# Kernel optimization log

Measured on AMD Instinct MI355X. Metric: run time of the kernel, lower is better.

The kernel has to match this reference:

```python
import jax, jax.numpy as jnp
import numpy as np

B, L_Q, S_KV, H, E = 4, 1024, 1024, 8, 64
IN_CH = OUT_CH = 512
MODES = 64
INDEX_Q = np.arange(MODES)   # 'lowest' mode selection -> range(0, modes)
INDEX_KV = np.arange(MODES)
SCALE = 1.0 / np.sqrt(OUT_CH)
FACTOR = 5


def setup_inputs() -> dict:
    key = jax.random.key(0)
    ks = jax.random.split(key, 7)
    tf_queries = jax.random.normal(ks[0], (B, L_Q, H, E), jnp.float32)
    queries = jax.random.normal(ks[1], (B, L_Q, H, E), jnp.float32)
    keys = jax.random.normal(ks[2], (B, S_KV, H, E), jnp.float32)
    values = jax.random.normal(ks[3], (B, S_KV, H, E), jnp.float32)
    mask = jnp.ones((1,), jnp.int32)  # unused by the module
    weights_fuse = jax.random.uniform(ks[4], (H, L_Q, 2), jnp.float32)
    # torch.rand with cfloat dtype samples re/im independently from U[0,1)
    w1_re = SCALE * jax.random.uniform(ks[5], (H, IN_CH // 8, OUT_CH // 8, MODES), jnp.float32)
    w1_im = SCALE * jax.random.uniform(ks[6], (H, IN_CH // 8, OUT_CH // 8, MODES), jnp.float32)
    return dict(tf_queries=tf_queries, queries=queries, keys=keys, values=values,
                mask=mask, weights_fuse=weights_fuse, w1_re=w1_re, w1_im=w1_im)


def get_sig_scores(n, queries, keys, scale, corr):
    # queries/keys: [B, L, H, E] (keys already aligned to L_Q)
    B_, Lq, H_, E_ = queries.shape
    Lk = keys.shape[1]
    q = jnp.transpose(queries, (0, 2, 1, 3))  # [B,H,L,E]
    k = jnp.transpose(keys, (0, 2, 1, 3))
    if corr:
        qf = jnp.fft.rfft(jnp.transpose(queries, (0, 2, 3, 1)), axis=-1)
        kf = jnp.fft.rfft(jnp.transpose(keys, (0, 2, 3, 1)), axis=-1)
        autocorr = jnp.transpose(jnp.fft.irfft(qf * jnp.conj(kf), axis=-1), (0, 1, 3, 2))  # [B,H,L,E]
    else:
        autocorr = q
    amp = jnp.linalg.norm(autocorr, axis=-1)           # [B,H,L]
    _, top_idx = jax.lax.top_k(amp, n)                 # [B,H,n]
    q_sel = jnp.take_along_axis(q, top_idx[..., None], axis=2)  # [B,H,n,E]
    scores = jnp.einsum('bhnd,bhmd->bhnm', q_sel, k) * scale    # [B,H,n,Lk]
    full = jnp.full((B_, H_, Lq, Lk), -jnp.inf, scores.dtype)
    bi = jnp.arange(B_)[:, None, None]
    hi = jnp.arange(H_)[None, :, None]
    full = full.at[bi, hi, top_idx].set(scores)        # scatter selected query rows
    # softmax over the query axis for every key position (transpose(2,3))
    return jax.nn.softmax(jnp.swapaxes(full, 2, 3), axis=-1)  # [B,H,Lk,Lq]


def reference(tf_queries, queries, keys, values, mask, weights_fuse, w1_re, w1_im):
    B_, Lq, H_, E_ = queries.shape
    S_ = keys.shape[1]
    xq = jnp.transpose(queries, (0, 2, 3, 1))  # [B,H,E,L_Q]
    xk = jnp.transpose(keys, (0, 2, 3, 1))     # [B,H,E,S]
    if Lq > S_:
        pad = jnp.zeros((B_, Lq - S_, H_, E_), keys.dtype)
        keys2 = jnp.concatenate([keys, pad], axis=1)
        values2 = jnp.concatenate([values, pad], axis=1)
    else:
        keys2 = keys[:, :Lq]
        values2 = values[:, :Lq]
    n_top = min(int(FACTOR * np.ceil(np.log(Lq))), Lq)

    attn_t = get_sig_scores(n_top, queries, keys2, SCALE, corr=True)
    attn_tf = get_sig_scores(n_top, tf_queries, keys2, SCALE, corr=False)

    nw = jax.nn.softmax(weights_fuse, axis=-1)  # [H,L_Q,2]
    fused = nw[None, :, :, 0, None] * attn_t + nw[None, :, :, 1, None] * attn_tf
    # dropout(p=0.1) in eval mode -> identity

    xq_ft = jnp.fft.rfft(xq, axis=-1)[:, :, :, INDEX_Q]   # [B,H,E,M]
    xk_ft = jnp.fft.rfft(xk, axis=-1)[:, :, :, INDEX_KV]  # [B,H,E,M]
    xqk = jnp.tanh(jnp.einsum('bhex,bhey->bhxy', xq_ft, xk_ft))  # complex tanh
    xqkv = jnp.einsum('bhxy,bhey->bhex', xqk, xk_ft)
    w1 = w1_re + 1j * w1_im
    xqkvw = jnp.einsum('bhex,heox->bhox', xqkv, w1)        # [B,H,O,M]
    out_ft = jnp.zeros((B_, H_, E_, Lq // 2 + 1), xqkvw.dtype)
    out_ft = out_ft.at[:, :, :, INDEX_Q].set(xqkvw)
    out = jnp.fft.irfft(out_ft / IN_CH / OUT_CH, n=Lq, axis=-1)  # [B,H,E,L_Q]

    output = jnp.einsum('bhlm,bhmd->bhld', fused, jnp.transpose(values2, (0, 2, 1, 3)))
    output = jnp.transpose(output, (0, 1, 3, 2))  # [B,H,D,L_Q]
    return (output + out) * 0.5
```

## Files before the change

kernel.cpp:

```cpp
#include <hip/hip_runtime.h>
#include <math.h>

#define B_ 4
#define H_ 8
#define L_ 1024
#define E_ 64
#define NTOP 35
#define SCALE_ 0.04419417382415922f

__global__ __launch_bounds__(256) void k_stage(const float* __restrict__ q_g,
                                               const float* __restrict__ k_g,
                                               float* __restrict__ xtq,
                                               float* __restrict__ xtk) {
  __shared__ float tile[64][65];
  const int tc = blockIdx.x & 15;
  const int src = (blockIdx.x >> 4) & 1;
  const int bh = blockIdx.x >> 5;
  const int b = bh >> 3, h = bh & 7;
  const int t0 = tc * 64;
  const int tid = threadIdx.x;
  const float* in = src ? k_g : q_g;
  float* out = src ? xtk : xtq;

  for (int idx = tid; idx < 1024; idx += 256) {
    int t = idx >> 4, e4 = idx & 15;
    float4 v = reinterpret_cast<const float4*>(
        in + ((size_t)(b * L_ + t0 + t) * H_ + h) * E_)[e4];
    tile[t][e4 * 4 + 0] = v.x; tile[t][e4 * 4 + 1] = v.y;
    tile[t][e4 * 4 + 2] = v.z; tile[t][e4 * 4 + 3] = v.w;
  }
  __syncthreads();
  for (int idx = tid; idx < 1024; idx += 256) {
    int e = idx >> 4, t4 = idx & 15;
    float4 v = make_float4(tile[t4 * 4 + 0][e], tile[t4 * 4 + 1][e],
                           tile[t4 * 4 + 2][e], tile[t4 * 4 + 3][e]);
    reinterpret_cast<float4*>(out + ((size_t)(bh * 64 + e)) * 1024 + t0)[t4] = v;
  }
}

__global__ __launch_bounds__(512) void k_fft_c(const float* __restrict__ xtq,
                                               const float* __restrict__ xtk,
                                               float* __restrict__ amp2_part,
                                               float* __restrict__ qft,
                                               float* __restrict__ kft) {
  __shared__ __align__(16) float zre[4][1024], zim[4][1024];
  __shared__ float ctab[512], stab[512];
  const int eg = blockIdx.x & 15;
  const int bh = blockIdx.x >> 4;
  const int tid = threadIdx.x;
  const float TWO_PI_N = 6.283185307179586f / 1024.0f;

  if (tid < 512) {
    float s, c;
    sincosf(TWO_PI_N * (float)tid, &s, &c);
    ctab[tid] = c; stab[tid] = s;
  }
  for (int idx = tid; idx < 1024; idx += 512) {
    int ee = idx >> 8, t4 = idx & 255;
    size_t ro = ((size_t)(bh * 64 + eg * 4 + ee)) * 1024;
    float4 qv = reinterpret_cast<const float4*>(xtq + ro)[t4];
    float4 kv = reinterpret_cast<const float4*>(xtk + ro)[t4];
    *reinterpret_cast<float4*>(&zre[ee][t4 * 4]) = qv;
    *reinterpret_cast<float4*>(&zim[ee][t4 * 4]) = kv;
  }
  __syncthreads();

  for (int s = 0; s < 10; ++s) {
    const int half = 512 >> s;
#pragma unroll
    for (int it = 0; it < 4; ++it) {
      int idx = tid + it * 512;
      int ee = idx >> 9;
      int bf = idx & 511;
      int j = bf & (half - 1);
      int p0 = ((bf >> (9 - s)) << (10 - s)) + j;
      int p1 = p0 + half;
      float ur = zre[ee][p0], ui = zim[ee][p0];
      float vr = zre[ee][p1], vi = zim[ee][p1];
      float dr = ur - vr, di = ui - vi;
      zre[ee][p0] = ur + vr; zim[ee][p0] = ui + vi;
      int twi = j << s;
      float c = ctab[twi], sn = stab[twi];
      zre[ee][p1] = fmaf(dr, c, di * sn);
      zim[ee][p1] = fmaf(di, c, -dr * sn);
    }
    __syncthreads();
  }

  float pr[8], pi_[8];
#pragma unroll
  for (int it = 0; it < 8; ++it) {
    int idx = tid + it * 512;
    int ee = idx >> 10;
    int p = idx & 1023;
    int m = __brev((unsigned)p) >> 22;
    int mp = (1024 - m) & 1023;
    int pp = __brev((unsigned)mp) >> 22;
    float ar = zre[ee][p], ai = zim[ee][p];
    float br = zre[ee][pp], bi = zim[ee][pp];
    float qr = 0.5f * (ar + br), qi = 0.5f * (ai - bi);
    float kr = 0.5f * (ai + bi), ki = -0.5f * (ar - br);
    pr[it]  = fmaf(qr, kr, qi * ki);
    pi_[it] = fmaf(qi, kr, -qr * ki);
    if (m < 64) {
      size_t o = ((size_t)(bh * 64 + eg * 4 + ee) * 64 + m) * 2;
      qft[o] = qr; qft[o + 1] = qi;
      kft[o] = kr; kft[o + 1] = ki;
    }
  }
  __syncthreads();
#pragma unroll
  for (int it = 0; it < 8; ++it) {
    int idx = tid + it * 512;
    int ee = idx >> 10;
    int p = idx & 1023;
    zre[ee][p] = pr[it]; zim[ee][p] = pi_[it];
  }
  __syncthreads();

  for (int idx = tid; idx < 2048; idx += 512) {
    int u = idx >> 10;
    int p = idx & 1023;
    int e0 = 2 * u, e1 = 2 * u + 1;
    float s_r = zre[e0][p] - zim[e1][p];
    float s_i = zim[e0][p] + zre[e1][p];
    zre[e0][p] = s_r; zim[e0][p] = s_i;
  }
  __syncthreads();

  for (int s = 9; s >= 0; --s) {
    const int half = 512 >> s;
#pragma unroll
    for (int it = 0; it < 2; ++it) {
      int idx = tid + it * 512;
      int ee = (idx >> 9) * 2;
      int bf = idx & 511;
      int j = bf & (half - 1);
      int p0 = ((bf >> (9 - s)) << (10 - s)) + j;
      int p1 = p0 + half;
      int twi = j << s;
      float c = ctab[twi], sn = stab[twi];
      float ur = zre[ee][p0], ui = zim[ee][p0];
      float wr = zre[ee][p1], wi = zim[ee][p1];
      float vr = fmaf(wr, c, -wi * sn);
      float vi = fmaf(wi, c, wr * sn);
      zre[ee][p0] = ur + vr; zim[ee][p0] = ui + vi;
      zre[ee][p1] = ur - vr; zim[ee][p1] = ui - vi;
    }
    __syncthreads();
  }

  for (int t = tid; t < 1024; t += 512) {
    float r0 = zre[0][t], i0 = zim[0][t];
    float r2 = zre[2][t], i2 = zim[2][t];
    amp2_part[(size_t)(bh * 16 + eg) * 1024 + t] =
        fmaf(r0, r0, fmaf(i0, i0, fmaf(r2, r2, i2 * i2)));
  }
}

__global__ __launch_bounds__(256) void k_fft_s(const float* __restrict__ q_g,
                                               const float* __restrict__ k_g,
                                               float* __restrict__ amp2_part,
                                               float* __restrict__ qft,
                                               float* __restrict__ kft) {
  __shared__ float zre[4][1024], zim[4][1024];
  __shared__ float ctab[512], stab[512];
  const int eg = blockIdx.x & 15;
  const int bh = blockIdx.x >> 4;
  const int b = bh >> 3, h = bh & 7;
  const int tid = threadIdx.x;
  const float TWO_PI_N = 6.283185307179586f / 1024.0f;

  for (int j = tid; j < 512; j += 256) {
    float s, c;
    sincosf(TWO_PI_N * (float)j, &s, &c);
    ctab[j] = c; stab[j] = s;
  }
  for (int t = tid; t < 1024; t += 256) {
    size_t g4 = ((size_t)(b * L_ + t) * H_ + h) * 16 + eg;
    float4 qv = reinterpret_cast<const float4*>(q_g)[g4];
    float4 kv = reinterpret_cast<const float4*>(k_g)[g4];
    zre[0][t] = qv.x; zre[1][t] = qv.y; zre[2][t] = qv.z; zre[3][t] = qv.w;
    zim[0][t] = kv.x; zim[1][t] = kv.y; zim[2][t] = kv.z; zim[3][t] = kv.w;
  }
  __syncthreads();

  for (int s = 0; s < 10; ++s) {
    const int half = 512 >> s;
#pragma unroll
    for (int it = 0; it < 8; ++it) {
      int idx = tid + it * 256;
      int ee = idx >> 9;
      int bf = idx & 511;
      int j = bf & (half - 1);
      int p0 = ((bf >> (9 - s)) << (10 - s)) + j;
      int p1 = p0 + half;
      float ur = zre[ee][p0], ui = zim[ee][p0];
      float vr = zre[ee][p1], vi = zim[ee][p1];
      float dr = ur - vr, di = ui - vi;
      zre[ee][p0] = ur + vr; zim[ee][p0] = ui + vi;
      int twi = j << s;
      float c = ctab[twi], sn = stab[twi];
      zre[ee][p1] = fmaf(dr, c, di * sn);
      zim[ee][p1] = fmaf(di, c, -dr * sn);
    }
    __syncthreads();
  }

  float pr[16], pi_[16];
#pragma unroll
  for (int it = 0; it < 16; ++it) {
    int idx = tid + it * 256;
    int ee = idx >> 10;
    int p = idx & 1023;
    int m = __brev((unsigned)p) >> 22;
    int mp = (1024 - m) & 1023;
    int pp = __brev((unsigned)mp) >> 22;
    float ar = zre[ee][p], ai = zim[ee][p];
    float br = zre[ee][pp], bi = zim[ee][pp];
    float qr = 0.5f * (ar + br), qi = 0.5f * (ai - bi);
    float kr = 0.5f * (ai + bi), ki = -0.5f * (ar - br);
    pr[it]  = fmaf(qr, kr, qi * ki);
    pi_[it] = fmaf(qi, kr, -qr * ki);
    if (m < 64) {
      size_t o = ((size_t)(bh * 64 + eg * 4 + ee) * 64 + m) * 2;
      qft[o] = qr; qft[o + 1] = qi;
      kft[o] = kr; kft[o + 1] = ki;
    }
  }
  __syncthreads();
#pragma unroll
  for (int it = 0; it < 16; ++it) {
    int idx = tid + it * 256;
    int ee = idx >> 10;
    int p = idx & 1023;
    zre[ee][p] = pr[it]; zim[ee][p] = pi_[it];
  }
  __syncthreads();

  for (int idx = tid; idx < 2048; idx += 256) {
    int u = idx >> 10;
    int p = idx & 1023;
    int e0 = 2 * u, e1 = 2 * u + 1;
    float s_r = zre[e0][p] - zim[e1][p];
    float s_i = zim[e0][p] + zre[e1][p];
    zre[e0][p] = s_r; zim[e0][p] = s_i;
  }
  __syncthreads();

  for (int s = 9; s >= 0; --s) {
    const int half = 512 >> s;
#pragma unroll
    for (int it = 0; it < 4; ++it) {
      int idx = tid + it * 256;
      int ee = (idx >> 9) * 2;
      int bf = idx & 511;
      int j = bf & (half - 1);
      int p0 = ((bf >> (9 - s)) << (10 - s)) + j;
      int p1 = p0 + half;
      int twi = j << s;
      float c = ctab[twi], sn = stab[twi];
      float ur = zre[ee][p0], ui = zim[ee][p0];
      float wr = zre[ee][p1], wi = zim[ee][p1];
      float vr = fmaf(wr, c, -wi * sn);
      float vi = fmaf(wi, c, wr * sn);
      zre[ee][p0] = ur + vr; zim[ee][p0] = ui + vi;
      zre[ee][p1] = ur - vr; zim[ee][p1] = ui - vi;
    }
    __syncthreads();
  }

  for (int t = tid; t < 1024; t += 256) {
    float r0 = zre[0][t], i0 = zim[0][t];
    float r2 = zre[2][t], i2 = zim[2][t];
    amp2_part[(size_t)(bh * 16 + eg) * 1024 + t] =
        fmaf(r0, r0, fmaf(i0, i0, fmaf(r2, r2, i2 * i2)));
  }
}

__global__ __launch_bounds__(256) void k_red(const float* __restrict__ amp2_part,
                                             const float* __restrict__ tfq,
                                             float* __restrict__ ampsum) {
  const int blk = blockIdx.x;
  const int tid = threadIdx.x;
  if (blk < 32) {
    const int bh = blk;
    for (int t = tid; t < 1024; t += 256) {
      float s = 0.f;
#pragma unroll
      for (int c = 0; c < 16; ++c)
        s += amp2_part[(size_t)(bh * 16 + c) * 1024 + t];
      ampsum[(size_t)(bh * 2) * 1024 + t] = s;
    }
  } else {
    const int idx = blk - 32;
    const int bh = idx >> 2, qt = idx & 3;
    const int b = bh >> 3, h = bh & 7;
    const int l = qt * 256 + tid;
    const float4* p4 = reinterpret_cast<const float4*>(
        &tfq[((size_t)(b * L_ + l) * H_ + h) * E_]);
    float s = 0.f;
#pragma unroll
    for (int e4 = 0; e4 < 16; ++e4) {
      float4 v = p4[e4];
      s += v.x * v.x + v.y * v.y + v.z * v.z + v.w * v.w;
    }
    ampsum[(size_t)(bh * 2 + 1) * 1024 + l] = s;
  }
}

__global__ __launch_bounds__(64) void k_sel(const float* __restrict__ ampsum,
                                            int* __restrict__ sel_ws) {
  const int p = blockIdx.x;
  const int lane = threadIdx.x;
  float val[16];
#pragma unroll
  for (int j = 0; j < 16; ++j)
    val[j] = ampsum[(size_t)p * 1024 + j * 64 + lane];

  float bv = -1.f; int bi = lane;
#pragma unroll
  for (int j = 0; j < 16; ++j) {
    if (val[j] > bv) { bv = val[j]; bi = j * 64 + lane; }
  }

  for (int it = 0; it < NTOP; ++it) {
    float v = bv; int i = bi;
#pragma unroll
    for (int d = 1; d < 64; d <<= 1) {
      float ov = __shfl_xor(v, d);
      int oi = __shfl_xor(i, d);
      if (ov > v || (ov == v && oi < i)) { v = ov; i = oi; }
    }
    if (lane == 0) sel_ws[p * 64 + it] = i;
    if ((i & 63) == lane) {
      int jr = i >> 6;
#pragma unroll
      for (int j = 0; j < 16; ++j) if (j == jr) val[j] = -1.f;
      bv = -1.f; bi = lane;
#pragma unroll
      for (int j = 0; j < 16; ++j) {
        if (val[j] > bv) { bv = val[j]; bi = j * 64 + lane; }
      }
    }
  }
}

__global__ __launch_bounds__(256) void k_topk(const float* __restrict__ amp2_part,
                                              const float* __restrict__ tfq,
                                              int* __restrict__ sel_ws) {
  __shared__ float amp[1024];
  __shared__ float wv_s[4];
  __shared__ int wi_s[4];
  __shared__ int winner_s;
  const int src = blockIdx.x & 1;
  const int bh = blockIdx.x >> 1;
  const int b = bh >> 3, h = bh & 7;
  const int tid = threadIdx.x;

  if (src == 0) {
    for (int t = tid; t < 1024; t += 256) {
      float s = 0.f;
#pragma unroll
      for (int c = 0; c < 16; ++c) s += amp2_part[(size_t)(bh * 16 + c) * 1024 + t];
      amp[t] = s;
    }
  } else {
    for (int l = tid; l < 1024; l += 256) {
      const float4* p4 = reinterpret_cast<const float4*>(
          &tfq[((size_t)(b * L_ + l) * H_ + h) * E_]);
      float s = 0.f;
#pragma unroll
      for (int e4 = 0; e4 < 16; ++e4) {
        float4 v = p4[e4];
        s += v.x * v.x + v.y * v.y + v.z * v.z + v.w * v.w;
      }
      amp[l] = s;
    }
  }
  __syncthreads();

  float bv = -1.f; int bi = tid;
#pragma unroll
  for (int kk = 0; kk < 4; ++kk) {
    int t = tid + kk * 256;
    float v = amp[t];
    if (v > bv) { bv = v; bi = t; }
  }
  const int lane = tid & 63, w = tid >> 6;

  for (int it = 0; it < NTOP; ++it) {
    float v = bv; int i = bi;
#pragma unroll
    for (int d = 1; d < 64; d <<= 1) {
      float ov = __shfl_xor(v, d);
      int oi = __shfl_xor(i, d);
      if (ov > v || (ov == v && oi < i)) { v = ov; i = oi; }
    }
    if (lane == 0) { wv_s[w] = v; wi_s[w] = i; }
    __syncthreads();
    if (tid == 0) {
      float fv = wv_s[0]; int fi = wi_s[0];
#pragma unroll
      for (int j = 1; j < 4; ++j) {
        if (wv_s[j] > fv || (wv_s[j] == fv && wi_s[j] < fi)) { fv = wv_s[j]; fi = wi_s[j]; }
      }
      winner_s = fi;
      sel_ws[(bh * 2 + src) * 64 + it] = fi;
    }
    __syncthreads();
    int fi = winner_s;
    if ((fi & 255) == tid) {
      amp[fi] = -1.f;
      bv = -1.f; bi = tid;
#pragma unroll
      for (int kk = 0; kk < 4; ++kk) {
        int t = tid + kk * 256;
        float vv = amp[t];
        if (vv > bv) { bv = vv; bi = t; }
      }
    }
  }
}

__global__ __launch_bounds__(256) void k_attn(const float* __restrict__ q_g,
                                              const float* __restrict__ tfq,
                                              const float* __restrict__ k_g,
                                              const float* __restrict__ v_g,
                                              const float* __restrict__ wfuse,
                                              const int* __restrict__ sel_ws,
                                              float* __restrict__ out) {
  __shared__ float4 qs4[2][NTOP][16];
  __shared__ float4 vs4[2][NTOP][16];
  const int ac = blockIdx.x & 15;
  const int bh = blockIdx.x >> 4;
  const int b = bh >> 3, h = bh & 7;
  const int a0 = ac * 64;
  const int tid = threadIdx.x;

  for (int idx = tid; idx < 2 * NTOP * 16; idx += 256) {
    int src = idx / (NTOP * 16);
    int rem = idx - src * (NTOP * 16);
    int i = rem >> 4, e4 = rem & 15;
    int row = sel_ws[(bh * 2 + src) * 64 + i];
    size_t rb = ((size_t)(b * L_ + row) * H_ + h) * E_;
    const float* qbase = src ? tfq : q_g;
    qs4[src][i][e4] = reinterpret_cast<const float4*>(qbase + rb)[e4];
    vs4[src][i][e4] = reinterpret_cast<const float4*>(v_g + rb)[e4];
  }
  __syncthreads();

  const int qd = tid & 3, r = tid >> 2;
  const int a = a0 + r;
  const int eb = qd * 16;

  size_t krb = ((size_t)(b * L_ + a) * H_ + h) * E_;
  const float4* k4p = reinterpret_cast<const float4*>(k_g + krb);
  float4 kq[4];
#pragma unroll
  for (int j4 = 0; j4 < 4; ++j4) kq[j4] = k4p[qd * 4 + j4];

  float ct[NTOP], ctf[NTOP];
#pragma unroll
  for (int i = 0; i < NTOP; ++i) { ct[i] = 0.f; ctf[i] = 0.f; }

#pragma unroll
  for (int j4 = 0; j4 < 4; ++j4) {
    float4 kv = kq[j4];
#pragma unroll
    for (int i = 0; i < NTOP; ++i) {
      float4 q4 = qs4[0][i][qd * 4 + j4];
      ct[i] = fmaf(q4.x, kv.x, ct[i]); ct[i] = fmaf(q4.y, kv.y, ct[i]);
      ct[i] = fmaf(q4.z, kv.z, ct[i]); ct[i] = fmaf(q4.w, kv.w, ct[i]);
      float4 p4 = qs4[1][i][qd * 4 + j4];
      ctf[i] = fmaf(p4.x, kv.x, ctf[i]); ctf[i] = fmaf(p4.y, kv.y, ctf[i]);
      ctf[i] = fmaf(p4.z, kv.z, ctf[i]); ctf[i] = fmaf(p4.w, kv.w, ctf[i]);
    }
  }
#pragma unroll
  for (int i = 0; i < NTOP; ++i) {
    ct[i] += __shfl_xor(ct[i], 1);  ct[i] += __shfl_xor(ct[i], 2);
    ctf[i] += __shfl_xor(ctf[i], 1); ctf[i] += __shfl_xor(ctf[i], 2);
  }

  float wf0 = wfuse[(h * L_ + a) * 2 + 0];
  float wf1 = wfuse[(h * L_ + a) * 2 + 1];
  float wm = fmaxf(wf0, wf1);
  float ew0 = expf(wf0 - wm), ew1 = expf(wf1 - wm);
  float nw0 = ew0 / (ew0 + ew1), nw1 = ew1 / (ew0 + ew1);

  {
    float m = -1e30f;
#pragma unroll
    for (int i = 0; i < NTOP; ++i) { ct[i] *= SCALE_; m = fmaxf(m, ct[i]); }
    float sum = 0.f;
#pragma unroll
    for (int i = 0; i < NTOP; ++i) { ct[i] = expf(ct[i] - m); sum += ct[i]; }
    float c = 0.5f * nw0 / sum;
#pragma unroll
    for (int i = 0; i < NTOP; ++i) ct[i] *= c;
  }
  {
    float m = -1e30f;
#pragma unroll
    for (int i = 0; i < NTOP; ++i) { ctf[i] *= SCALE_; m = fmaxf(m, ctf[i]); }
    float sum = 0.f;
#pragma unroll
    for (int i = 0; i < NTOP; ++i) { ctf[i] = expf(ctf[i] - m); sum += ctf[i]; }
    float c = 0.5f * nw1 / sum;
#pragma unroll
    for (int i = 0; i < NTOP; ++i) ctf[i] *= c;
  }
#pragma unroll
  for (int j4 = 0; j4 < 4; ++j4) {
    float ax = 0.f, ay = 0.f, az = 0.f, aw = 0.f;
#pragma unroll
    for (int i = 0; i < NTOP; ++i) {
      float4 v4 = vs4[0][i][qd * 4 + j4];
      ax = fmaf(ct[i], v4.x, ax); ay = fmaf(ct[i], v4.y, ay);
      az = fmaf(ct[i], v4.z, az); aw = fmaf(ct[i], v4.w, aw);
    }
#pragma unroll
    for (int i = 0; i < NTOP; ++i) {
      float4 v4 = vs4[1][i][qd * 4 + j4];
      ax = fmaf(ctf[i], v4.x, ax); ay = fmaf(ctf[i], v4.y, ay);
      az = fmaf(ctf[i], v4.z, az); aw = fmaf(ctf[i], v4.w, aw);
    }
    int d = eb + j4 * 4;
    out[((size_t)(bh * 64 + d + 0)) * 1024 + a] = ax;
    out[((size_t)(bh * 64 + d + 1)) * 1024 + a] = ay;
    out[((size_t)(bh * 64 + d + 2)) * 1024 + a] = az;
    out[((size_t)(bh * 64 + d + 3)) * 1024 + a] = aw;
  }
}

__global__ __launch_bounds__(256) void k_spec12(const float* __restrict__ qft,
                                                 const float* __restrict__ kft,
                                                 float* __restrict__ xre_g,
                                                 float* __restrict__ xim_g) {
  __shared__ float kre[64][65], kim[64][65];
  __shared__ float qre[64][8], qim[64][8];
  __shared__ float tre[8][64], tim[8][64];
  const int xc = blockIdx.x & 7;
  const int bh = blockIdx.x >> 3;
  const int tid = threadIdx.x;

  for (int idx = tid; idx < 4096; idx += 256) {
    int e = idx >> 6, y = idx & 63;
    size_t o = ((size_t)(bh * 64 + e) * 64 + y) * 2;
    kre[e][y] = kft[o]; kim[e][y] = kft[o + 1];
  }
  for (int idx = tid; idx < 512; idx += 256) {
    int e = idx >> 3, xl = idx & 7;
    size_t o = ((size_t)(bh * 64 + e) * 64 + xc * 8 + xl) * 2;
    qre[e][xl] = qft[o]; qim[e][xl] = qft[o + 1];
  }
  __syncthreads();

  const int y = tid & 63, xg = tid >> 6;
#pragma unroll
  for (int xi = 0; xi < 2; ++xi) {
    int xl = xg + xi * 4;
    float ar = 0.f, ai = 0.f;
    for (int e = 0; e < 64; ++e) {
      float a = qre[e][xl], b = qim[e][xl];
      float c = kre[e][y], d = kim[e][y];
      ar = fmaf(a, c, fmaf(-b, d, ar));
      ai = fmaf(a, d, fmaf(b, c, ai));
    }
    float trv, tiv;
    float x2 = 2.f * ar, y2 = 2.f * ai;
    if (fabsf(x2) > 30.f) {
      trv = copysignf(1.f, ar); tiv = 0.f;
    } else {
      float sh = sinhf(x2), ch = coshf(x2);
      float sn = sinf(y2), cs = cosf(y2);
      float dd = ch + cs;
      trv = sh / dd; tiv = sn / dd;
    }
    tre[xl][y] = trv; tim[xl][y] = tiv;
  }
  __syncthreads();

  const int e2 = tid & 63, xg2 = tid >> 6;
#pragma unroll
  for (int xi = 0; xi < 2; ++xi) {
    int xl = xg2 + xi * 4;
    float ar = 0.f, ai = 0.f;
    for (int yy = 0; yy < 64; ++yy) {
      float a = tre[xl][yy], b = tim[xl][yy];
      float c = kre[e2][yy], d = kim[e2][yy];
      ar = fmaf(a, c, fmaf(-b, d, ar));
      ai = fmaf(a, d, fmaf(b, c, ai));
    }
    xre_g[(size_t)bh * 4096 + (xc * 8 + xl) * 64 + e2] = ar;
    xim_g[(size_t)bh * 4096 + (xc * 8 + xl) * 64 + e2] = ai;
  }
}

__global__ __launch_bounds__(256) void k_w1(const float* __restrict__ xre_g,
                                            const float* __restrict__ xim_g,
                                            const float* __restrict__ w1re,
                                            const float* __restrict__ w1im,
                                            float* __restrict__ xw) {
  __shared__ float xre[64][65], xim[64][65];
  __shared__ float redr[4][512], redi[4][512];
  const int oc = blockIdx.x & 7;
  const int bh = blockIdx.x >> 3;
  const int h = bh & 7;
  const int tid = threadIdx.x;

  for (int idx = tid; idx < 4096; idx += 256) {
    int x = idx >> 6, e = idx & 63;
    xre[e][x] = xre_g[(size_t)bh * 4096 + idx];
    xim[e][x] = xim_g[(size_t)bh * 4096 + idx];
  }
  __syncthreads();

  const int x = tid & 63, g = tid >> 6;
  float accr[8], acci[8];
#pragma unroll
  for (int oo = 0; oo < 8; ++oo) { accr[oo] = 0.f; acci[oo] = 0.f; }

  for (int ee = 0; ee < 16; ++ee) {
    int e = g * 16 + ee;
    float a = xre[e][x], b = xim[e][x];
    size_t wbase = (((size_t)h * 64 + e) * 64 + oc * 8) * 64 + x;
#pragma unroll
    for (int oo = 0; oo < 8; ++oo) {
      float c = w1re[wbase + (size_t)oo * 64];
      float d = w1im[wbase + (size_t)oo * 64];
      accr[oo] = fmaf(a, c, fmaf(-b, d, accr[oo]));
      acci[oo] = fmaf(a, d, fmaf(b, c, acci[oo]));
    }
  }
#pragma unroll
  for (int oo = 0; oo < 8; ++oo) {
    redr[g][oo * 64 + x] = accr[oo];
    redi[g][oo * 64 + x] = acci[oo];
  }
  __syncthreads();

  const float INV = 1.0f / (512.0f * 512.0f);
  for (int idx = tid; idx < 512; idx += 256) {
    int oo = idx >> 6, x2 = idx & 63;
    float r = redr[0][idx] + redr[1][idx] + redr[2][idx] + redr[3][idx];
    float i = redi[0][idx] + redi[1][idx] + redi[2][idx] + redi[3][idx];
    size_t oidx = ((size_t)(bh * 64 + oc * 8 + oo) * 64 + x2) * 2;
    xw[oidx] = r * INV;
    xw[oidx + 1] = i * INV;
  }
}

__global__ __launch_bounds__(256) void k_final(const float* __restrict__ xw,
                                               float* __restrict__ out) {
  __shared__ float Xre[8][64], Xim[8][64];
  const int tc = blockIdx.x & 3;
  const int oc = (blockIdx.x >> 2) & 7;
  const int bh = blockIdx.x >> 5;
  const int o0 = oc * 8;
  const int tid = threadIdx.x;

  for (int idx = tid; idx < 512; idx += 256) {
    int o = idx >> 6, m = idx & 63;
    size_t s = ((size_t)(bh * 64 + o0 + o) * 64 + m) * 2;
    Xre[o][m] = 2.f * xw[s]; Xim[o][m] = 2.f * xw[s + 1];
  }
  __syncthreads();

  const int t = tc * 256 + tid;
  const float HALF_INVN = 0.5f / 1024.0f;
  const float TWO_PI = 6.283185307179586f;
  float th = TWO_PI * (float)t * (1.0f / 1024.0f);
  float s1, c1;
  __sincosf(th, &s1, &c1);
  float cm = c1, sm = s1;

  float acc[8];
#pragma unroll
  for (int o = 0; o < 8; ++o) acc[o] = 0.5f * Xre[o][0];

  for (int m = 1; m < 64; ++m) {
#pragma unroll
    for (int o = 0; o < 8; ++o) {
      acc[o] = fmaf(Xre[o][m], cm, acc[o]);
      acc[o] = fmaf(-Xim[o][m], sm, acc[o]);
    }
    float cn = fmaf(cm, c1, -sm * s1);
    float sn = fmaf(sm, c1, cm * s1);
    cm = cn; sm = sn;
  }
#pragma unroll
  for (int o = 0; o < 8; ++o) {
    size_t oi = ((size_t)(bh * 64 + o0 + o)) * 1024 + t;
    out[oi] = fmaf(acc[o], HALF_INVN, out[oi]);
  }
}

extern "C" void kernel_launch(void* const* d_in, const int* in_sizes, int n_in,
                              void* d_out, int out_size, void* d_ws, size_t ws_size,
                              hipStream_t stream) {
  const float* tfq   = (const float*)d_in[0];
  const float* q     = (const float*)d_in[1];
  const float* k     = (const float*)d_in[2];
  const float* v     = (const float*)d_in[3];
  const float* wfuse = (const float*)d_in[5];
  const float* w1re  = (const float*)d_in[6];
  const float* w1im  = (const float*)d_in[7];
  float* out = (float*)d_out;
  float* ws  = (float*)d_ws;

  const size_t STAGED_FLOATS = 5312512;
  if (ws_size >= STAGED_FLOATS * sizeof(float)) {
    float* xtq    = ws;
    float* xtk    = ws + 2097152;
    float* amp2   = ws + 4194304;
    float* qft    = ws + 4718592;
    float* kft    = ws + 4980736;
    int*   sel    = (int*)(ws + 5242880);
    float* ampsum = ws + 5246976;
    float* xre_g  = ws;
    float* xim_g  = ws + 131072;
    float* xw     = ws + 262144;

    k_stage<<<1024, 256, 0, stream>>>(q, k, xtq, xtk);
    k_fft_c<<<512, 512, 0, stream>>>(xtq, xtk, amp2, qft, kft);
    k_red<<<160, 256, 0, stream>>>(amp2, tfq, ampsum);
    k_sel<<<64, 64, 0, stream>>>(ampsum, sel);
    k_attn<<<512, 256, 0, stream>>>(q, tfq, k, v, wfuse, sel, out);
    k_spec12<<<256, 256, 0, stream>>>(qft, kft, xre_g, xim_g);
    k_w1<<<256, 256, 0, stream>>>(xre_g, xim_g, w1re, w1im, xw);
    k_final<<<1024, 256, 0, stream>>>(xw, out);
  } else {
    float* amp2  = ws;
    float* xre_g = ws;
    float* xim_g = ws + 131072;
    float* xw    = ws + 262144;
    float* qft   = ws + 524288;
    float* kft   = ws + 786432;
    int*   sel   = (int*)(ws + 1048576);

    k_fft_s<<<512, 256, 0, stream>>>(q, k, amp2, qft, kft);
    k_topk<<<64, 256, 0, stream>>>(amp2, tfq, sel);
    k_attn<<<512, 256, 0, stream>>>(q, tfq, k, v, wfuse, sel, out);
    k_spec12<<<256, 256, 0, stream>>>(qft, kft, xre_g, xim_g);
    k_w1<<<256, 256, 0, stream>>>(xre_g, xim_g, w1re, w1im, xw);
    k_final<<<1024, 256, 0, stream>>>(xw, out);
  }
}
```

Measured before the change: 134.0 us.

## Merge independent stages into five launches via virtual-block dispatch

Kernel bodies become device functions that take a virtual block id and a shared scratch buffer. Independent stages then share one launch: staging runs with the tfq norm, the amp reduction and top-k run with spec12, and attention runs with the w1 projection. The launch count in the staged path drops from eight to five, which cuts launch gaps and lets independent work fill the GPU together. In exchange, each fused launch reserves shared memory for its largest stage, which may lower occupancy for the smaller stages.

Result: faster. 114.0 us (-14.9%).

```diff
diff --git a/kernel.cpp b/kernel.cpp
--- a/kernel.cpp
+++ b/kernel.cpp
@@ -8,14 +8,16 @@
 #define NTOP 35
 #define SCALE_ 0.04419417382415922f
 
-__global__ __launch_bounds__(256) void k_stage(const float* __restrict__ q_g,
-                                               const float* __restrict__ k_g,
-                                               float* __restrict__ xtq,
-                                               float* __restrict__ xtk) {
-  __shared__ float tile[64][65];
-  const int tc = blockIdx.x & 15;
-  const int src = (blockIdx.x >> 4) & 1;
-  const int bh = blockIdx.x >> 5;
+
+__device__ __forceinline__ void dev_stage(char* smem, int vbid,
+                                          const float* __restrict__ q_g,
+                                          const float* __restrict__ k_g,
+                                          float* __restrict__ xtq,
+                                          float* __restrict__ xtk) {
+  float* tile = reinterpret_cast<float*>(smem);
+  const int tc = vbid & 15;
+  const int src = (vbid >> 4) & 1;
+  const int bh = vbid >> 5;
   const int b = bh >> 3, h = bh & 7;
   const int t0 = tc * 64;
   const int tid = threadIdx.x;
@@ -26,27 +28,47 @@
     int t = idx >> 4, e4 = idx & 15;
     float4 v = reinterpret_cast<const float4*>(
         in + ((size_t)(b * L_ + t0 + t) * H_ + h) * E_)[e4];
-    tile[t][e4 * 4 + 0] = v.x; tile[t][e4 * 4 + 1] = v.y;
-    tile[t][e4 * 4 + 2] = v.z; tile[t][e4 * 4 + 3] = v.w;
+    tile[t * 65 + e4 * 4 + 0] = v.x; tile[t * 65 + e4 * 4 + 1] = v.y;
+    tile[t * 65 + e4 * 4 + 2] = v.z; tile[t * 65 + e4 * 4 + 3] = v.w;
   }
   __syncthreads();
   for (int idx = tid; idx < 1024; idx += 256) {
     int e = idx >> 4, t4 = idx & 15;
-    float4 v = make_float4(tile[t4 * 4 + 0][e], tile[t4 * 4 + 1][e],
-                           tile[t4 * 4 + 2][e], tile[t4 * 4 + 3][e]);
+    float4 v = make_float4(tile[(t4 * 4 + 0) * 65 + e], tile[(t4 * 4 + 1) * 65 + e],
+                           tile[(t4 * 4 + 2) * 65 + e], tile[(t4 * 4 + 3) * 65 + e]);
     reinterpret_cast<float4*>(out + ((size_t)(bh * 64 + e)) * 1024 + t0)[t4] = v;
   }
 }
 
-__global__ __launch_bounds__(512) void k_fft_c(const float* __restrict__ xtq,
-                                               const float* __restrict__ xtk,
-                                               float* __restrict__ amp2_part,
-                                               float* __restrict__ qft,
-                                               float* __restrict__ kft) {
-  __shared__ __align__(16) float zre[4][1024], zim[4][1024];
-  __shared__ float ctab[512], stab[512];
-  const int eg = blockIdx.x & 15;
-  const int bh = blockIdx.x >> 4;
+__device__ __forceinline__ void dev_tfqnorm(int vbid,
+                                            const float* __restrict__ tfq,
+                                            float* __restrict__ ampsum) {
+  const int bh = vbid >> 2, qt = vbid & 3;
+  const int b = bh >> 3, h = bh & 7;
+  const int l = qt * 256 + threadIdx.x;
+  const float4* p4 = reinterpret_cast<const float4*>(
+      &tfq[((size_t)(b * L_ + l) * H_ + h) * E_]);
+  float s = 0.f;
+#pragma unroll
+  for (int e4 = 0; e4 < 16; ++e4) {
+    float4 v = p4[e4];
+    s += v.x * v.x + v.y * v.y + v.z * v.z + v.w * v.w;
+  }
+  ampsum[(size_t)(bh * 2 + 1) * 1024 + l] = s;
+}
+
+__device__ __forceinline__ void dev_fft(char* smem, int vbid,
+                                        const float* __restrict__ xtq,
+                                        const float* __restrict__ xtk,
+                                        float* __restrict__ amp2_part,
+                                        float* __restrict__ qft,
+                                        float* __restrict__ kft) {
+  float* zre = reinterpret_cast<float*>(smem);
+  float* zim = zre + 4096;
+  float* ctab = zim + 4096;
+  float* stab = ctab + 512;
+  const int eg = vbid & 15;
+  const int bh = vbid >> 4;
   const int tid = threadIdx.x;
   const float TWO_PI_N = 6.283185307179586f / 1024.0f;
 
@@ -60,8 +82,8 @@
     size_t ro = ((size_t)(bh * 64 + eg * 4 + ee)) * 1024;
     float4 qv = reinterpret_cast<const float4*>(xtq + ro)[t4];
     float4 kv = reinterpret_cast<const float4*>(xtk + ro)[t4];
-    *reinterpret_cast<float4*>(&zre[ee][t4 * 4]) = qv;
-    *reinterpret_cast<float4*>(&zim[ee][t4 * 4]) = kv;
+    *reinterpret_cast<float4*>(&zre[ee * 1024 + t4 * 4]) = qv;
+    *reinterpret_cast<float4*>(&zim[ee * 1024 + t4 * 4]) = kv;
   }
   __syncthreads();
 
@@ -75,14 +97,14 @@
       int j = bf & (half - 1);
       int p0 = ((bf >> (9 - s)) << (10 - s)) + j;
       int p1 = p0 + half;
-      float ur = zre[ee][p0], ui = zim[ee][p0];
-      float vr = zre[ee][p1], vi = zim[ee][p1];
+      float ur = zre[ee * 1024 + p0], ui = zim[ee * 1024 + p0];
+      float vr = zre[ee * 1024 + p1], vi = zim[ee * 1024 + p1];
       float dr = ur - vr, di = ui - vi;
-      zre[ee][p0] = ur + vr; zim[ee][p0] = ui + vi;
+      zre[ee * 1024 + p0] = ur + vr; zim[ee * 1024 + p0] = ui + vi;
       int twi = j << s;
       float c = ctab[twi], sn = stab[twi];
-      zre[ee][p1] = fmaf(dr, c, di * sn);
-      zim[ee][p1] = fmaf(di, c, -dr * sn);
+      zre[ee * 1024 + p1] = fmaf(dr, c, di * sn);
+      zim[ee * 1024 + p1] = fmaf(di, c, -dr * sn);
     }
     __syncthreads();
   }
@@ -96,8 +118,8 @@
     int m = __brev((unsigned)p) >> 22;
     int mp = (1024 - m) & 1023;
     int pp = __brev((unsigned)mp) >> 22;
-    float ar = zre[ee][p], ai = zim[ee][p];
-    float br = zre[ee][pp], bi = zim[ee][pp];
+    float ar = zre[ee * 1024 + p], ai = zim[ee * 1024 + p];
+    float br = zre[ee * 1024 + pp], bi = zim[ee * 1024 + pp];
     float qr = 0.5f * (ar + br), qi = 0.5f * (ai - bi);
     float kr = 0.5f * (ai + bi), ki = -0.5f * (ar - br);
     pr[it]  = fmaf(qr, kr, qi * ki);
@@ -114,7 +136,7 @@
     int idx = tid + it * 512;
     int ee = idx >> 10;
     int p = idx & 1023;
-    zre[ee][p] = pr[it]; zim[ee][p] = pi_[it];
+    zre[ee * 1024 + p] = pr[it]; zim[ee * 1024 + p] = pi_[it];
   }
   __syncthreads();
 
@@ -122,9 +144,9 @@
     int u = idx >> 10;
     int p = idx & 1023;
     int e0 = 2 * u, e1 = 2 * u + 1;
-    float s_r = zre[e0][p] - zim[e1][p];
-    float s_i = zim[e0][p] + zre[e1][p];
-    zre[e0][p] = s_r; zim[e0][p] = s_i;
+    float s_r = zre[e0 * 1024 + p] - zim[e1 * 1024 + p];
+    float s_i = zim[e0 * 1024 + p] + zre[e1 * 1024 + p];
+    zre[e0 * 1024 + p] = s_r; zim[e0 * 1024 + p] = s_i;
   }
   __syncthreads();
 
@@ -140,23 +162,421 @@
       int p1 = p0 + half;
       int twi = j << s;
       float c = ctab[twi], sn = stab[twi];
-      float ur = zre[ee][p0], ui = zim[ee][p0];
-      float wr = zre[ee][p1], wi = zim[ee][p1];
+      float ur = zre[ee * 1024 + p0], ui = zim[ee * 1024 + p0];
+      float wr = zre[ee * 1024 + p1], wi = zim[ee * 1024 + p1];
       float vr = fmaf(wr, c, -wi * sn);
       float vi = fmaf(wi, c, wr * sn);
-      zre[ee][p0] = ur + vr; zim[ee][p0] = ui + vi;
-      zre[ee][p1] = ur - vr; zim[ee][p1] = ui - vi;
+      zre[ee * 1024 + p0] = ur + vr; zim[ee * 1024 + p0] = ui + vi;
+      zre[ee * 1024 + p1] = ur - vr; zim[ee * 1024 + p1] = ui - vi;
     }
     __syncthreads();
   }
 
   for (int t = tid; t < 1024; t += 512) {
-    float r0 = zre[0][t], i0 = zim[0][t];
-    float r2 = zre[2][t], i2 = zim[2][t];
+    float r0 = zre[t], i0 = zim[t];
+    float r2 = zre[2 * 1024 + t], i2 = zim[2 * 1024 + t];
     amp2_part[(size_t)(bh * 16 + eg) * 1024 + t] =
         fmaf(r0, r0, fmaf(i0, i0, fmaf(r2, r2, i2 * i2)));
   }
 }
+
+__device__ __forceinline__ void dev_sel(char* smem, int vbid,
+                                        const float* __restrict__ amp2_part,
+                                        const float* __restrict__ ampsum,
+                                        int* __restrict__ sel_ws) {
+  float* amp = reinterpret_cast<float*>(smem);
+  const int p = vbid;
+  const int tid = threadIdx.x;
+
+  if ((p & 1) == 0) {
+    const int bh = p >> 1;
+    for (int t = tid; t < 1024; t += 256) {
+      float s = 0.f;
+#pragma unroll
+      for (int c = 0; c < 16; ++c)
+        s += amp2_part[(size_t)(bh * 16 + c) * 1024 + t];
+      amp[t] = s;
+    }
+  } else {
+    for (int t = tid; t < 1024; t += 256)
+      amp[t] = ampsum[(size_t)p * 1024 + t];
+  }
+  __syncthreads();
+
+  if (tid < 64) {
+    const int lane = tid;
+    float val[16];
+#pragma unroll
+    for (int j = 0; j < 16; ++j) val[j] = amp[j * 64 + lane];
+
+    float bv = -1.f; int bi = lane;
+#pragma unroll
+    for (int j = 0; j < 16; ++j) {
+      if (val[j] > bv) { bv = val[j]; bi = j * 64 + lane; }
+    }
+    for (int it = 0; it < NTOP; ++it) {
+      float v = bv; int i = bi;
+#pragma unroll
+      for (int d = 1; d < 64; d <<= 1) {
+        float ov = __shfl_xor(v, d);
+        int oi = __shfl_xor(i, d);
+        if (ov > v || (ov == v && oi < i)) { v = ov; i = oi; }
+      }
+      if (lane == 0) sel_ws[p * 64 + it] = i;
+      if ((i & 63) == lane) {
+        int jr = i >> 6;
+#pragma unroll
+        for (int j = 0; j < 16; ++j) if (j == jr) val[j] = -1.f;
+        bv = -1.f; bi = lane;
+#pragma unroll
+        for (int j = 0; j < 16; ++j) {
+          if (val[j] > bv) { bv = val[j]; bi = j * 64 + lane; }
+        }
+      }
+    }
+  }
+}
+
+__device__ __forceinline__ void dev_attn(char* smem, int vbid,
+                                         const float* __restrict__ q_g,
+                                         const float* __restrict__ tfq,
+                                         const float* __restrict__ k_g,
+                                         const float* __restrict__ v_g,
+                                         const float* __restrict__ wfuse,
+                                         const int* __restrict__ sel_ws,
+                                         float* __restrict__ out) {
+  float4* qs4 = reinterpret_cast<float4*>(smem);
+  float4* vs4 = qs4 + 2 * NTOP * 16;
+  const int ac = vbid & 15;
+  const int bh = vbid >> 4;
+  const int b = bh >> 3, h = bh & 7;
+  const int a0 = ac * 64;
+  const int tid = threadIdx.x;
+
+  for (int idx = tid; idx < 2 * NTOP * 16; idx += 256) {
+    int src = idx / (NTOP * 16);
+    int rem = idx - src * (NTOP * 16);
+    int i = rem >> 4, e4 = rem & 15;
+    int row = sel_ws[(bh * 2 + src) * 64 + i];
+    size_t rb = ((size_t)(b * L_ + row) * H_ + h) * E_;
+    const float* qbase = src ? tfq : q_g;
+    qs4[(src * NTOP + i) * 16 + e4] = reinterpret_cast<const float4*>(qbase + rb)[e4];
+    vs4[(src * NTOP + i) * 16 + e4] = reinterpret_cast<const float4*>(v_g + rb)[e4];
+  }
+  __syncthreads();
+
+  const int qd = tid & 3, r = tid >> 2;
+  const int a = a0 + r;
+  const int eb = qd * 16;
+
+  size_t krb = ((size_t)(b * L_ + a) * H_ + h) * E_;
+  const float4* k4p = reinterpret_cast<const float4*>(k_g + krb);
+  float4 kq[4];
+#pragma unroll
+  for (int j4 = 0; j4 < 4; ++j4) kq[j4] = k4p[qd * 4 + j4];
+
+  float ct[NTOP], ctf[NTOP];
+#pragma unroll
+  for (int i = 0; i < NTOP; ++i) { ct[i] = 0.f; ctf[i] = 0.f; }
+
+#pragma unroll
+  for (int j4 = 0; j4 < 4; ++j4) {
+    float4 kv = kq[j4];
+#pragma unroll
+    for (int i = 0; i < NTOP; ++i) {
+      float4 q4 = qs4[(0 * NTOP + i) * 16 + qd * 4 + j4];
+      ct[i] = fmaf(q4.x, kv.x, ct[i]); ct[i] = fmaf(q4.y, kv.y, ct[i]);
+      ct[i] = fmaf(q4.z, kv.z, ct[i]); ct[i] = fmaf(q4.w, kv.w, ct[i]);
+      float4 p4 = qs4[(1 * NTOP + i) * 16 + qd * 4 + j4];
+      ctf[i] = fmaf(p4.x, kv.x, ctf[i]); ctf[i] = fmaf(p4.y, kv.y, ctf[i]);
+      ctf[i] = fmaf(p4.z, kv.z, ctf[i]); ctf[i] = fmaf(p4.w, kv.w, ctf[i]);
+    }
+  }
+#pragma unroll
+  for (int i = 0; i < NTOP; ++i) {
+    ct[i] += __shfl_xor(ct[i], 1);  ct[i] += __shfl_xor(ct[i], 2);
+    ctf[i] += __shfl_xor(ctf[i], 1); ctf[i] += __shfl_xor(ctf[i], 2);
+  }
+
+  float wf0 = wfuse[(h * L_ + a) * 2 + 0];
+  float wf1 = wfuse[(h * L_ + a) * 2 + 1];
+  float wm = fmaxf(wf0, wf1);
+  float ew0 = expf(wf0 - wm), ew1 = expf(wf1 - wm);
+  float nw0 = ew0 / (ew0 + ew1), nw1 = ew1 / (ew0 + ew1);
+
+  {
+    float m = -1e30f;
+#pragma unroll
+    for (int i = 0; i < NTOP; ++i) { ct[i] *= SCALE_; m = fmaxf(m, ct[i]); }
+    float sum = 0.f;
+#pragma unroll
+    for (int i = 0; i < NTOP; ++i) { ct[i] = expf(ct[i] - m); sum += ct[i]; }
+    float c = 0.5f * nw0 / sum;
+#pragma unroll
+    for (int i = 0; i < NTOP; ++i) ct[i] *= c;
+  }
+  {
+    float m = -1e30f;
+#pragma unroll
+    for (int i = 0; i < NTOP; ++i) { ctf[i] *= SCALE_; m = fmaxf(m, ctf[i]); }
+    float sum = 0.f;
+#pragma unroll
+    for (int i = 0; i < NTOP; ++i) { ctf[i] = expf(ctf[i] - m); sum += ctf[i]; }
+    float c = 0.5f * nw1 / sum;
+#pragma unroll
+    for (int i = 0; i < NTOP; ++i) ctf[i] *= c;
+  }
+#pragma unroll
+  for (int j4 = 0; j4 < 4; ++j4) {
+    float ax = 0.f, ay = 0.f, az = 0.f, aw = 0.f;
+#pragma unroll
+    for (int i = 0; i < NTOP; ++i) {
+      float4 v4 = vs4[(0 * NTOP + i) * 16 + qd * 4 + j4];
+      ax = fmaf(ct[i], v4.x, ax); ay = fmaf(ct[i], v4.y, ay);
+      az = fmaf(ct[i], v4.z, az); aw = fmaf(ct[i], v4.w, aw);
+    }
+#pragma unroll
+    for (int i = 0; i < NTOP; ++i) {
+      float4 v4 = vs4[(1 * NTOP + i) * 16 + qd * 4 + j4];
+      ax = fmaf(ctf[i], v4.x, ax); ay = fmaf(ctf[i], v4.y, ay);
+      az = fmaf(ctf[i], v4.z, az); aw = fmaf(ctf[i], v4.w, aw);
+    }
+    int d = eb + j4 * 4;
+    out[((size_t)(bh * 64 + d + 0)) * 1024 + a] = ax;
+    out[((size_t)(bh * 64 + d + 1)) * 1024 + a] = ay;
+    out[((size_t)(bh * 64 + d + 2)) * 1024 + a] = az;
+    out[((size_t)(bh * 64 + d + 3)) * 1024 + a] = aw;
+  }
+}
+
+__device__ __forceinline__ void dev_spec12(char* smem, int vbid,
+                                           const float* __restrict__ qft,
+                                           const float* __restrict__ kft,
+                                           float* __restrict__ xre_g,
+                                           float* __restrict__ xim_g) {
+  float* kre = reinterpret_cast<float*>(smem);
+  float* kim = kre + 4160;
+  float* qre = kim + 4160;
+  float* qim = qre + 512;
+  float* tre = qim + 512;
+  float* tim = tre + 512;
+  const int xc = vbid & 7;
+  const int bh = vbid >> 3;
+  const int tid = threadIdx.x;
+
+  for (int idx = tid; idx < 4096; idx += 256) {
+    int e = idx >> 6, y = idx & 63;
+    size_t o = ((size_t)(bh * 64 + e) * 64 + y) * 2;
+    kre[e * 65 + y] = kft[o]; kim[e * 65 + y] = kft[o + 1];
+  }
+  for (int idx = tid; idx < 512; idx += 256) {
+    int e = idx >> 3, xl = idx & 7;
+    size_t o = ((size_t)(bh * 64 + e) * 64 + xc * 8 + xl) * 2;
+    qre[e * 8 + xl] = qft[o]; qim[e * 8 + xl] = qft[o + 1];
+  }
+  __syncthreads();
+
+  const int y = tid & 63, xg = tid >> 6;
+#pragma unroll
+  for (int xi = 0; xi < 2; ++xi) {
+    int xl = xg + xi * 4;
+    float ar = 0.f, ai = 0.f;
+    for (int e = 0; e < 64; ++e) {
+      float a = qre[e * 8 + xl], b = qim[e * 8 + xl];
+      float c = kre[e * 65 + y], d = kim[e * 65 + y];
+      ar = fmaf(a, c, fmaf(-b, d, ar));
+      ai = fmaf(a, d, fmaf(b, c, ai));
+    }
+    float trv, tiv;
+    float x2 = 2.f * ar, y2 = 2.f * ai;
+    if (fabsf(x2) > 30.f) {
+      trv = copysignf(1.f, ar); tiv = 0.f;
+    } else {
+      float sh = sinhf(x2), ch = coshf(x2);
+      float sn = sinf(y2), cs = cosf(y2);
+      float dd = ch + cs;
+      trv = sh / dd; tiv = sn / dd;
+    }
+    tre[xl * 64 + y] = trv; tim[xl * 64 + y] = tiv;
+  }
+  __syncthreads();
+
+  const int e2 = tid & 63, xg2 = tid >> 6;
+#pragma unroll
+  for (int xi = 0; xi < 2; ++xi) {
+    int xl = xg2 + xi * 4;
+    float ar = 0.f, ai = 0.f;
+    for (int yy = 0; yy < 64; ++yy) {
+      float a = tre[xl * 64 + yy], b = tim[xl * 64 + yy];
+      float c = kre[e2 * 65 + yy], d = kim[e2 * 65 + yy];
+      ar = fmaf(a, c, fmaf(-b, d, ar));
+      ai = fmaf(a, d, fmaf(b, c, ai));
+    }
+    xre_g[(size_t)bh * 4096 + (xc * 8 + xl) * 64 + e2] = ar;
+    xim_g[(size_t)bh * 4096 + (xc * 8 + xl) * 64 + e2] = ai;
+  }
+}
+
+__device__ __forceinline__ void dev_w1(char* smem, int vbid,
+                                       const float* __restrict__ xre_g,
+                                       const float* __restrict__ xim_g,
+                                       const float* __restrict__ w1re,
+                                       const float* __restrict__ w1im,
+                                       float* __restrict__ xw) {
+  float* xre = reinterpret_cast<float*>(smem);
+  float* xim = xre + 4160;
+  float* redr = xim + 4160;
+  float* redi = redr + 2048;
+  const int oc = vbid & 7;
+  const int bh = vbid >> 3;
+  const int h = bh & 7;
+  const int tid = threadIdx.x;
+
+  for (int idx = tid; idx < 4096; idx += 256) {
+    int x = idx >> 6, e = idx & 63;
+    xre[e * 65 + x] = xre_g[(size_t)bh * 4096 + idx];
+    xim[e * 65 + x] = xim_g[(size_t)bh * 4096 + idx];
+  }
+  __syncthreads();
+
+  const int x = tid & 63, g = tid >> 6;
+  float accr[8], acci[8];
+#pragma unroll
+  for (int oo = 0; oo < 8; ++oo) { accr[oo] = 0.f; acci[oo] = 0.f; }
+
+  for (int ee = 0; ee < 16; ++ee) {
+    int e = g * 16 + ee;
+    float a = xre[e * 65 + x], b = xim[e * 65 + x];
+    size_t wbase = (((size_t)h * 64 + e) * 64 + oc * 8) * 64 + x;
+#pragma unroll
+    for (int oo = 0; oo < 8; ++oo) {
+      float c = w1re[wbase + (size_t)oo * 64];
+      float d = w1im[wbase + (size_t)oo * 64];
+      accr[oo] = fmaf(a, c, fmaf(-b, d, accr[oo]));
+      acci[oo] = fmaf(a, d, fmaf(b, c, acci[oo]));
+    }
+  }
+#pragma unroll
+  for (int oo = 0; oo < 8; ++oo) {
+    redr[g * 512 + oo * 64 + x] = accr[oo];
+    redi[g * 512 + oo * 64 + x] = acci[oo];
+  }
+  __syncthreads();
+
+  const float INV = 1.0f / (512.0f * 512.0f);
+  for (int idx = tid; idx < 512; idx += 256) {
+    int oo = idx >> 6, x2 = idx & 63;
+    float r = redr[idx] + redr[512 + idx] + redr[1024 + idx] + redr[1536 + idx];
+    float i = redi[idx] + redi[512 + idx] + redi[1024 + idx] + redi[1536 + idx];
+    size_t oidx = ((size_t)(bh * 64 + oc * 8 + oo) * 64 + x2) * 2;
+    xw[oidx] = r * INV;
+    xw[oidx + 1] = i * INV;
+  }
+}
+
+__device__ __forceinline__ void dev_final(char* smem, int vbid,
+                                          const float* __restrict__ xw,
+                                          float* __restrict__ out) {
+  float* Xre = reinterpret_cast<float*>(smem);
+  float* Xim = Xre + 512;
+  const int tc = vbid & 3;
+  const int oc = (vbid >> 2) & 7;
+  const int bh = vbid >> 5;
+  const int o0 = oc * 8;
+  const int tid = threadIdx.x;
+
+  for (int idx = tid; idx < 512; idx += 256) {
+    int o = idx >> 6, m = idx & 63;
+    size_t s = ((size_t)(bh * 64 + o0 + o) * 64 + m) * 2;
+    Xre[o * 64 + m] = 2.f * xw[s]; Xim[o * 64 + m] = 2.f * xw[s + 1];
+  }
+  __syncthreads();
+
+  const int t = tc * 256 + tid;
+  const float HALF_INVN = 0.5f / 1024.0f;
+  const float TWO_PI = 6.283185307179586f;
+  float th = TWO_PI * (float)t * (1.0f / 1024.0f);
+  float s1, c1;
+  __sincosf(th, &s1, &c1);
+  float cm = c1, sm = s1;
+
+  float acc[8];
+#pragma unroll
+  for (int o = 0; o < 8; ++o) acc[o] = 0.5f * Xre[o * 64];
+
+  for (int m = 1; m < 64; ++m) {
+#pragma unroll
+    for (int o = 0; o < 8; ++o) {
+      acc[o] = fmaf(Xre[o * 64 + m], cm, acc[o]);
+      acc[o] = fmaf(-Xim[o * 64 + m], sm, acc[o]);
+    }
+    float cn = fmaf(cm, c1, -sm * s1);
+    float sn = fmaf(sm, c1, cm * s1);
+    cm = cn; sm = sn;
+  }
+#pragma unroll
+  for (int o = 0; o < 8; ++o) {
+    size_t oi = ((size_t)(bh * 64 + o0 + o)) * 1024 + t;
+    out[oi] = fmaf(acc[o], HALF_INVN, out[oi]);
+  }
+}
+
+
+__global__ __launch_bounds__(256) void k_L1(const float* __restrict__ q,
+                                            const float* __restrict__ k,
+                                            const float* __restrict__ tfq,
+                                            float* __restrict__ xtq,
+                                            float* __restrict__ xtk,
+                                            float* __restrict__ ampsum) {
+  __shared__ __align__(16) char smem[16640];
+  if (blockIdx.x < 1024) dev_stage(smem, blockIdx.x, q, k, xtq, xtk);
+  else dev_tfqnorm(blockIdx.x - 1024, tfq, ampsum);
+}
+
+__global__ __launch_bounds__(512) void k_L2(const float* __restrict__ xtq,
+                                            const float* __restrict__ xtk,
+                                            float* __restrict__ amp2,
+                                            float* __restrict__ qft,
+                                            float* __restrict__ kft) {
+  __shared__ __align__(16) char smem[36864];
+  dev_fft(smem, blockIdx.x, xtq, xtk, amp2, qft, kft);
+}
+
+__global__ __launch_bounds__(256) void k_L3(const float* __restrict__ amp2,
+                                            const float* __restrict__ ampsum,
+                                            int* __restrict__ sel,
+                                            const float* __restrict__ qft,
+                                            const float* __restrict__ kft,
+                                            float* __restrict__ xre_g,
+                                            float* __restrict__ xim_g) {
+  __shared__ __align__(16) char smem[41472];
+  if (blockIdx.x < 64) dev_sel(smem, blockIdx.x, amp2, ampsum, sel);
+  else dev_spec12(smem, blockIdx.x - 64, qft, kft, xre_g, xim_g);
+}
+
+__global__ __launch_bounds__(256) void k_L4(const float* __restrict__ q,
+                                            const float* __restrict__ tfq,
+                                            const float* __restrict__ k,
+                                            const float* __restrict__ v,
+                                            const float* __restrict__ wfuse,
+                                            const int* __restrict__ sel,
+                                            float* __restrict__ out,
+                                            const float* __restrict__ xre_g,
+                                            const float* __restrict__ xim_g,
+                                            const float* __restrict__ w1re,
+                                            const float* __restrict__ w1im,
+                                            float* __restrict__ xw) {
+  __shared__ __align__(16) char smem[49664];
+  if (blockIdx.x < 512) dev_attn(smem, blockIdx.x, q, tfq, k, v, wfuse, sel, out);
+  else dev_w1(smem, blockIdx.x - 512, xre_g, xim_g, w1re, w1im, xw);
+}
+
+__global__ __launch_bounds__(256) void k_L5(const float* __restrict__ xw,
+                                            float* __restrict__ out) {
+  __shared__ __align__(16) char smem[4096];
+  dev_final(smem, blockIdx.x, xw, out);
+}
+
 
 __global__ __launch_bounds__(256) void k_fft_s(const float* __restrict__ q_g,
                                                const float* __restrict__ k_g,
@@ -278,74 +698,6 @@
   }
 }
 
-__global__ __launch_bounds__(256) void k_red(const float* __restrict__ amp2_part,
-                                             const float* __restrict__ tfq,
-                                             float* __restrict__ ampsum) {
-  const int blk = blockIdx.x;
-  const int tid = threadIdx.x;
-  if (blk < 32) {
-    const int bh = blk;
-    for (int t = tid; t < 1024; t += 256) {
-      float s = 0.f;
-#pragma unroll
-      for (int c = 0; c < 16; ++c)
-        s += amp2_part[(size_t)(bh * 16 + c) * 1024 + t];
-      ampsum[(size_t)(bh * 2) * 1024 + t] = s;
-    }
-  } else {
-    const int idx = blk - 32;
-    const int bh = idx >> 2, qt = idx & 3;
-    const int b = bh >> 3, h = bh & 7;
-    const int l = qt * 256 + tid;
-    const float4* p4 = reinterpret_cast<const float4*>(
-        &tfq[((size_t)(b * L_ + l) * H_ + h) * E_]);
-    float s = 0.f;
-#pragma unroll
-    for (int e4 = 0; e4 < 16; ++e4) {
-      float4 v = p4[e4];
-      s += v.x * v.x + v.y * v.y + v.z * v.z + v.w * v.w;
-    }
-    ampsum[(size_t)(bh * 2 + 1) * 1024 + l] = s;
-  }
-}
-
-__global__ __launch_bounds__(64) void k_sel(const float* __restrict__ ampsum,
-                                            int* __restrict__ sel_ws) {
-  const int p = blockIdx.x;
-  const int lane = threadIdx.x;
-  float val[16];
-#pragma unroll
-  for (int j = 0; j < 16; ++j)
-    val[j] = ampsum[(size_t)p * 1024 + j * 64 + lane];
-
-  float bv = -1.f; int bi = lane;
-#pragma unroll
-  for (int j = 0; j < 16; ++j) {
-    if (val[j] > bv) { bv = val[j]; bi = j * 64 + lane; }
-  }
-
-  for (int it = 0; it < NTOP; ++it) {
-    float v = bv; int i = bi;
-#pragma unroll
-    for (int d = 1; d < 64; d <<= 1) {
-      float ov = __shfl_xor(v, d);
-      int oi = __shfl_xor(i, d);
-      if (ov > v || (ov == v && oi < i)) { v = ov; i = oi; }
-    }
-    if (lane == 0) sel_ws[p * 64 + it] = i;
-    if ((i & 63) == lane) {
-      int jr = i >> 6;
-#pragma unroll
-      for (int j = 0; j < 16; ++j) if (j == jr) val[j] = -1.f;
-      bv = -1.f; bi = lane;
-#pragma unroll
-      for (int j = 0; j < 16; ++j) {
-        if (val[j] > bv) { bv = val[j]; bi = j * 64 + lane; }
-      }
-    }
-  }
-}
-
 __global__ __launch_bounds__(256) void k_topk(const float* __restrict__ amp2_part,
                                               const float* __restrict__ tfq,
                                               int* __restrict__ sel_ws) {
@@ -423,278 +775,32 @@
   }
 }
 
-__global__ __launch_bounds__(256) void k_attn(const float* __restrict__ q_g,
-                                              const float* __restrict__ tfq,
-                                              const float* __restrict__ k_g,
-                                              const float* __restrict__ v_g,
-                                              const float* __restrict__ wfuse,
-                                              const int* __restrict__ sel_ws,
-                                              float* __restrict__ out) {
-  __shared__ float4 qs4[2][NTOP][16];
-  __shared__ float4 vs4[2][NTOP][16];
-  const int ac = blockIdx.x & 15;
-  const int bh = blockIdx.x >> 4;
-  const int b = bh >> 3, h = bh & 7;
-  const int a0 = ac * 64;
-  const int tid = threadIdx.x;
-
-  for (int idx = tid; idx < 2 * NTOP * 16; idx += 256) {
-    int src = idx / (NTOP * 16);
-    int rem = idx - src * (NTOP * 16);
-    int i = rem >> 4, e4 = rem & 15;
-    int row = sel_ws[(bh * 2 + src) * 64 + i];
-    size_t rb = ((size_t)(b * L_ + row) * H_ + h) * E_;
-    const float* qbase = src ? tfq : q_g;
-    qs4[src][i][e4] = reinterpret_cast<const float4*>(qbase + rb)[e4];
-    vs4[src][i][e4] = reinterpret_cast<const float4*>(v_g + rb)[e4];
-  }
-  __syncthreads();
-
-  const int qd = tid & 3, r = tid >> 2;
-  const int a = a0 + r;
-  const int eb = qd * 16;
-
-  size_t krb = ((size_t)(b * L_ + a) * H_ + h) * E_;
-  const float4* k4p = reinterpret_cast<const float4*>(k_g + krb);
-  float4 kq[4];
-#pragma unroll
-  for (int j4 = 0; j4 < 4; ++j4) kq[j4] = k4p[qd * 4 + j4];
-
-  float ct[NTOP], ctf[NTOP];
-#pragma unroll
-  for (int i = 0; i < NTOP; ++i) { ct[i] = 0.f; ctf[i] = 0.f; }
-
-#pragma unroll
-  for (int j4 = 0; j4 < 4; ++j4) {
-    float4 kv = kq[j4];
-#pragma unroll
-    for (int i = 0; i < NTOP; ++i) {
-      float4 q4 = qs4[0][i][qd * 4 + j4];
-      ct[i] = fmaf(q4.x, kv.x, ct[i]); ct[i] = fmaf(q4.y, kv.y, ct[i]);
-      ct[i] = fmaf(q4.z, kv.z, ct[i]); ct[i] = fmaf(q4.w, kv.w, ct[i]);
-      float4 p4 = qs4[1][i][qd * 4 + j4];
-      ctf[i] = fmaf(p4.x, kv.x, ctf[i]); ctf[i] = fmaf(p4.y, kv.y, ctf[i]);
-      ctf[i] = fmaf(p4.z, kv.z, ctf[i]); ctf[i] = fmaf(p4.w, kv.w, ctf[i]);
-    }
-  }
-#pragma unroll
-  for (int i = 0; i < NTOP; ++i) {
-    ct[i] += __shfl_xor(ct[i], 1);  ct[i] += __shfl_xor(ct[i], 2);
-    ctf[i] += __shfl_xor(ctf[i], 1); ctf[i] += __shfl_xor(ctf[i], 2);
-  }
-
-  float wf0 = wfuse[(h * L_ + a) * 2 + 0];
-  float wf1 = wfuse[(h * L_ + a) * 2 + 1];
-  float wm = fmaxf(wf0, wf1);
-  float ew0 = expf(wf0 - wm), ew1 = expf(wf1 - wm);
-  float nw0 = ew0 / (ew0 + ew1), nw1 = ew1 / (ew0 + ew1);
-
-  {
-    float m = -1e30f;
-#pragma unroll
-    for (int i = 0; i < NTOP; ++i) { ct[i] *= SCALE_; m = fmaxf(m, ct[i]); }
-    float sum = 0.f;
-#pragma unroll
-    for (int i = 0; i < NTOP; ++i) { ct[i] = expf(ct[i] - m); sum += ct[i]; }
-    float c = 0.5f * nw0 / sum;
-#pragma unroll
-    for (int i = 0; i < NTOP; ++i) ct[i] *= c;
-  }
-  {
-    float m = -1e30f;
-#pragma unroll
-    for (int i = 0; i < NTOP; ++i) { ctf[i] *= SCALE_; m = fmaxf(m, ctf[i]); }
-    float sum = 0.f;
-#pragma unroll
-    for (int i = 0; i < NTOP; ++i) { ctf[i] = expf(ctf[i] - m); sum += ctf[i]; }
-    float c = 0.5f * nw1 / sum;
-#pragma unroll
-    for (int i = 0; i < NTOP; ++i) ctf[i] *= c;
-  }
-#pragma unroll
-  for (int j4 = 0; j4 < 4; ++j4) {
-    float ax = 0.f, ay = 0.f, az = 0.f, aw = 0.f;
-#pragma unroll
-    for (int i = 0; i < NTOP; ++i) {
-      float4 v4 = vs4[0][i][qd * 4 + j4];
-      ax = fmaf(ct[i], v4.x, ax); ay = fmaf(ct[i], v4.y, ay);
-      az = fmaf(ct[i], v4.z, az); aw = fmaf(ct[i], v4.w, aw);
-    }
-#pragma unroll
-    for (int i = 0; i < NTOP; ++i) {
-      float4 v4 = vs4[1][i][qd * 4 + j4];
-      ax = fmaf(ctf[i], v4.x, ax); ay = fmaf(ctf[i], v4.y, ay);
-      az = fmaf(ctf[i], v4.z, az); aw = fmaf(ctf[i], v4.w, aw);
-    }
-    int d = eb + j4 * 4;
-    out[((size_t)(bh * 64 + d + 0)) * 1024 + a] = ax;
-    out[((size_t)(bh * 64 + d + 1)) * 1024 + a] = ay;
-    out[((size_t)(bh * 64 + d + 2)) * 1024 + a] = az;
-    out[((size_t)(bh * 64 + d + 3)) * 1024 + a] = aw;
-  }
-}
-
-__global__ __launch_bounds__(256) void k_spec12(const float* __restrict__ qft,
-                                                 const float* __restrict__ kft,
-                                                 float* __restrict__ xre_g,
-                                                 float* __restrict__ xim_g) {
-  __shared__ float kre[64][65], kim[64][65];
-  __shared__ float qre[64][8], qim[64][8];
-  __shared__ float tre[8][64], tim[8][64];
-  const int xc = blockIdx.x & 7;
-  const int bh = blockIdx.x >> 3;
-  const int tid = threadIdx.x;
-
-  for (int idx = tid; idx < 4096; idx += 256) {
-    int e = idx >> 6, y = idx & 63;
-    size_t o = ((size_t)(bh * 64 + e) * 64 + y) * 2;
-    kre[e][y] = kft[o]; kim[e][y] = kft[o + 1];
-  }
-  for (int idx = tid; idx < 512; idx += 256) {
-    int e = idx >> 3, xl = idx & 7;
-    size_t o = ((size_t)(bh * 64 + e) * 64 + xc * 8 + xl) * 2;
-    qre[e][xl] = qft[o]; qim[e][xl] = qft[o + 1];
-  }
-  __syncthreads();
-
-  const int y = tid & 63, xg = tid >> 6;
-#pragma unroll
-  for (int xi = 0; xi < 2; ++xi) {
-    int xl = xg + xi * 4;
-    float ar = 0.f, ai = 0.f;
-    for (int e = 0; e < 64; ++e) {
-      float a = qre[e][xl], b = qim[e][xl];
-      float c = kre[e][y], d = kim[e][y];
-      ar = fmaf(a, c, fmaf(-b, d, ar));
-      ai = fmaf(a, d, fmaf(b, c, ai));
-    }
-    float trv, tiv;
-    float x2 = 2.f * ar, y2 = 2.f * ai;
-    if (fabsf(x2) > 30.f) {
-      trv = copysignf(1.f, ar); tiv = 0.f;
-    } else {
-      float sh = sinhf(x2), ch = coshf(x2);
-      float sn = sinf(y2), cs = cosf(y2);
-      float dd = ch + cs;
-      trv = sh / dd; tiv = sn / dd;
-    }
-    tre[xl][y] = trv; tim[xl][y] = tiv;
-  }
-  __syncthreads();
-
-  const int e2 = tid & 63, xg2 = tid >> 6;
-#pragma unroll
-  for (int xi = 0; xi < 2; ++xi) {
-    int xl = xg2 + xi * 4;
-    float ar = 0.f, ai = 0.f;
-    for (int yy = 0; yy < 64; ++yy) {
-      float a = tre[xl][yy], b = tim[xl][yy];
-      float c = kre[e2][yy], d = kim[e2][yy];
-      ar = fmaf(a, c, fmaf(-b, d, ar));
-      ai = fmaf(a, d, fmaf(b, c, ai));
-    }
-    xre_g[(size_t)bh * 4096 + (xc * 8 + xl) * 64 + e2] = ar;
-    xim_g[(size_t)bh * 4096 + (xc * 8 + xl) * 64 + e2] = ai;
-  }
-}
-
-__global__ __launch_bounds__(256) void k_w1(const float* __restrict__ xre_g,
-                                            const float* __restrict__ xim_g,
-                                            const float* __restrict__ w1re,
-                                            const float* __restrict__ w1im,
-                                            float* __restrict__ xw) {
-  __shared__ float xre[64][65], xim[64][65];
-  __shared__ float redr[4][512], redi[4][512];
-  const int oc = blockIdx.x & 7;
-  const int bh = blockIdx.x >> 3;
-  const int h = bh & 7;
-  const int tid = threadIdx.x;
-
-  for (int idx = tid; idx < 4096; idx += 256) {
-    int x = idx >> 6, e = idx & 63;
-    xre[e][x] = xre_g[(size_t)bh * 4096 + idx];
-    xim[e][x] = xim_g[(size_t)bh * 4096 + idx];
-  }
-  __syncthreads();
-
-  const int x = tid & 63, g = tid >> 6;
-  float accr[8], acci[8];
-#pragma unroll
-  for (int oo = 0; oo < 8; ++oo) { accr[oo] = 0.f; acci[oo] = 0.f; }
-
-  for (int ee = 0; ee < 16; ++ee) {
-    int e = g * 16 + ee;
-    float a = xre[e][x], b = xim[e][x];
-    size_t wbase = (((size_t)h * 64 + e) * 64 + oc * 8) * 64 + x;
-#pragma unroll
-    for (int oo = 0; oo < 8; ++oo) {
-      float c = w1re[wbase + (size_t)oo * 64];
-      float d = w1im[wbase + (size_t)oo * 64];
-      accr[oo] = fmaf(a, c, fmaf(-b, d, accr[oo]));
-      acci[oo] = fmaf(a, d, fmaf(b, c, acci[oo]));
-    }
-  }
-#pragma unroll
-  for (int oo = 0; oo < 8; ++oo) {
-    redr[g][oo * 64 + x] = accr[oo];
-    redi[g][oo * 64 + x] = acci[oo];
-  }
-  __syncthreads();
-
-  const float INV = 1.0f / (512.0f * 512.0f);
-  for (int idx = tid; idx < 512; idx += 256) {
-    int oo = idx >> 6, x2 = idx & 63;
-    float r = redr[0][idx] + redr[1][idx] + redr[2][idx] + redr[3][idx];
-    float i = redi[0][idx] + redi[1][idx] + redi[2][idx] + redi[3][idx];
-    size_t oidx = ((size_t)(bh * 64 + oc * 8 + oo) * 64 + x2) * 2;
-    xw[oidx] = r * INV;
-    xw[oidx + 1] = i * INV;
-  }
-}
-
-__global__ __launch_bounds__(256) void k_final(const float* __restrict__ xw,
-                                               float* __restrict__ out) {
-  __shared__ float Xre[8][64], Xim[8][64];
-  const int tc = blockIdx.x & 3;
-  const int oc = (blockIdx.x >> 2) & 7;
-  const int bh = blockIdx.x >> 5;
-  const int o0 = oc * 8;
-  const int tid = threadIdx.x;
-
-  for (int idx = tid; idx < 512; idx += 256) {
-    int o = idx >> 6, m = idx & 63;
-    size_t s = ((size_t)(bh * 64 + o0 + o) * 64 + m) * 2;
-    Xre[o][m] = 2.f * xw[s]; Xim[o][m] = 2.f * xw[s + 1];
-  }
-  __syncthreads();
-
-  const int t = tc * 256 + tid;
-  const float HALF_INVN = 0.5f / 1024.0f;
-  const float TWO_PI = 6.283185307179586f;
-  float th = TWO_PI * (float)t * (1.0f / 1024.0f);
-  float s1, c1;
-  __sincosf(th, &s1, &c1);
-  float cm = c1, sm = s1;
-
-  float acc[8];
-#pragma unroll
-  for (int o = 0; o < 8; ++o) acc[o] = 0.5f * Xre[o][0];
-
-  for (int m = 1; m < 64; ++m) {
-#pragma unroll
-    for (int o = 0; o < 8; ++o) {
-      acc[o] = fmaf(Xre[o][m], cm, acc[o]);
-      acc[o] = fmaf(-Xim[o][m], sm, acc[o]);
-    }
-    float cn = fmaf(cm, c1, -sm * s1);
-    float sn = fmaf(sm, c1, cm * s1);
-    cm = cn; sm = sn;
-  }
-#pragma unroll
-  for (int o = 0; o < 8; ++o) {
-    size_t oi = ((size_t)(bh * 64 + o0 + o)) * 1024 + t;
-    out[oi] = fmaf(acc[o], HALF_INVN, out[oi]);
-  }
+__global__ __launch_bounds__(256) void k_attn_w(const float* __restrict__ q,
+                                                const float* __restrict__ tfq,
+                                                const float* __restrict__ k,
+                                                const float* __restrict__ v,
+                                                const float* __restrict__ wfuse,
+                                                const int* __restrict__ sel,
+                                                float* __restrict__ out) {
+  __shared__ __align__(16) char smem[35840];
+  dev_attn(smem, blockIdx.x, q, tfq, k, v, wfuse, sel, out);
+}
+
+__global__ __launch_bounds__(256) void k_spec12_w(const float* __restrict__ qft,
+                                                  const float* __restrict__ kft,
+                                                  float* __restrict__ xre_g,
+                                                  float* __restrict__ xim_g) {
+  __shared__ __align__(16) char smem[41472];
+  dev_spec12(smem, blockIdx.x, qft, kft, xre_g, xim_g);
+}
+
+__global__ __launch_bounds__(256) void k_w1_w(const float* __restrict__ xre_g,
+                                              const float* __restrict__ xim_g,
+                                              const float* __restrict__ w1re,
+                                              const float* __restrict__ w1im,
+                                              float* __restrict__ xw) {
+  __shared__ __align__(16) char smem[49664];
+  dev_w1(smem, blockIdx.x, xre_g, xim_g, w1re, w1im, xw);
 }
 
 extern "C" void kernel_launch(void* const* d_in, const int* in_sizes, int n_in,
@@ -723,14 +829,12 @@
     float* xim_g  = ws + 131072;
     float* xw     = ws + 262144;
 
-    k_stage<<<1024, 256, 0, stream>>>(q, k, xtq, xtk);
-    k_fft_c<<<512, 512, 0, stream>>>(xtq, xtk, amp2, qft, kft);
-    k_red<<<160, 256, 0, stream>>>(amp2, tfq, ampsum);
-    k_sel<<<64, 64, 0, stream>>>(ampsum, sel);
-    k_attn<<<512, 256, 0, stream>>>(q, tfq, k, v, wfuse, sel, out);
-    k_spec12<<<256, 256, 0, stream>>>(qft, kft, xre_g, xim_g);
-    k_w1<<<256, 256, 0, stream>>>(xre_g, xim_g, w1re, w1im, xw);
-    k_final<<<1024, 256, 0, stream>>>(xw, out);
+    k_L1<<<1152, 256, 0, stream>>>(q, k, tfq, xtq, xtk, ampsum);
+    k_L2<<<512, 512, 0, stream>>>(xtq, xtk, amp2, qft, kft);
+    k_L3<<<320, 256, 0, stream>>>(amp2, ampsum, sel, qft, kft, xre_g, xim_g);
+    k_L4<<<768, 256, 0, stream>>>(q, tfq, k, v, wfuse, sel, out,
+                                  xre_g, xim_g, w1re, w1im, xw);
+    k_L5<<<1024, 256, 0, stream>>>(xw, out);
   } else {
     float* amp2  = ws;
     float* xre_g = ws;
@@ -742,9 +846,9 @@
 
     k_fft_s<<<512, 256, 0, stream>>>(q, k, amp2, qft, kft);
     k_topk<<<64, 256, 0, stream>>>(amp2, tfq, sel);
-    k_attn<<<512, 256, 0, stream>>>(q, tfq, k, v, wfuse, sel, out);
-    k_spec12<<<256, 256, 0, stream>>>(qft, kft, xre_g, xim_g);
-    k_w1<<<256, 256, 0, stream>>>(xre_g, xim_g, w1re, w1im, xw);
-    k_final<<<1024, 256, 0, stream>>>(xw, out);
-  }
-}
+    k_attn_w<<<512, 256, 0, stream>>>(q, tfq, k, v, wfuse, sel, out);
+    k_spec12_w<<<256, 256, 0, stream>>>(qft, kft, xre_g, xim_g);
+    k_w1_w<<<256, 256, 0, stream>>>(xre_g, xim_g, w1re, w1im, xw);
+    k_L5<<<1024, 256, 0, stream>>>(xw, out);
+  }
+}
```
